# Kernel optimization log

Measured on AMD Instinct MI355X. Metric: run time of the kernel, lower is better.

Reference implementation:

```python
import jax, jax.numpy as jnp
import numpy as np

B, S, D, H = 2, 2048, 1024, 16
HD = D // H  # head_dim = 64


def setup_inputs() -> dict:
    key = jax.random.key(0)
    ks = jax.random.split(key, 10)
    s = 1.0 / np.sqrt(D)
    # causal mask: 0 on/below diagonal, -inf above (matches masked_fill(mask == -inf))
    neg_inf = jnp.float32(-jnp.inf)
    mask = jnp.where(jnp.tril(jnp.ones((S, S), dtype=bool)), 0.0, neg_inf).astype(jnp.float32)
    return {
        "x": jax.random.normal(ks[0], (B, S, D), dtype=jnp.float32),
        "mask": mask,
        "Wq": jax.random.uniform(ks[1], (D, D), jnp.float32, -s, s),
        "bq": jax.random.uniform(ks[2], (D,), jnp.float32, -s, s),
        "Wk": jax.random.uniform(ks[3], (D, D), jnp.float32, -s, s),
        "bk": jax.random.uniform(ks[4], (D,), jnp.float32, -s, s),
        "Wv": jax.random.uniform(ks[5], (D, D), jnp.float32, -s, s),
        "bv": jax.random.uniform(ks[6], (D,), jnp.float32, -s, s),
        "Wo": jax.random.uniform(ks[7], (D, D), jnp.float32, -s, s),
        "bo": jax.random.uniform(ks[8], (D,), jnp.float32, -s, s),
    }


def reference(x, mask, Wq, bq, Wk, bk, Wv, bv, Wo, bo):
    b, s, d = x.shape
    scale = jnp.float32(HD) ** 0.5
    # qkv projections (torch Linear: y = x W^T + b), split into heads: [b, H, s, hd]
    q = (x @ Wq.T + bq).reshape(b, s, H, HD).transpose(0, 2, 1, 3)
    k = (x @ Wk.T + bk).reshape(b, s, H, HD).transpose(0, 2, 1, 3)
    v = (x @ Wv.T + bv).reshape(b, s, H, HD).transpose(0, 2, 1, 3)
    scores = jnp.einsum("bhqd,bhkd->bhqk", q, k) / scale
    scores = jnp.where(mask[None, None] == -jnp.inf, -jnp.inf, scores)
    attn = jax.nn.softmax(scores, axis=-1)
    # dropout(p=0.1) is identity in eval mode
    ctx = jnp.einsum("bhqk,bhkd->bhqd", attn, v)
    ctx = ctx.transpose(0, 2, 1, 3).reshape(b, s, d)
    return ctx @ Wo.T + bo
```

## Files before the change

kernel.cpp:

```cpp
#include <hip/hip_runtime.h>
#include <hip/hip_bf16.h>
#include <cmath>

#define S_ 2048
#define D_ 1024
#define H_ 16
#define HD_ 64
#define GM 4096
#define GN 1024
#define GK 1024
#define QSCALE 0.1803368801111f
#define THR2   11.5415603f

typedef __attribute__((ext_vector_type(4))) float f32x4;
typedef __attribute__((ext_vector_type(8))) short bf16x8;
typedef __attribute__((ext_vector_type(4))) short bf16x4;

__device__ __forceinline__ short f2bf(float f) {
    union { float f; unsigned u; } x; x.f = f;
    unsigned r = x.u + 0x7fffu + ((x.u >> 16) & 1u);
    return (short)(r >> 16);
}
__device__ __forceinline__ short bftrunc(float f) {
    union { float f; unsigned u; } x; x.f = f;
    return (short)(x.u >> 16);
}
__device__ __forceinline__ void gload16(const short* g, short* l) {
    __builtin_amdgcn_global_load_lds((const __attribute__((address_space(1))) void*)g,
                                     (__attribute__((address_space(3))) void*)l, 16, 0, 0);
}

__global__ __launch_bounds__(256) void cvt_all(
    const float* __restrict__ x,
    const float* __restrict__ w0, const float* __restrict__ w1,
    const float* __restrict__ w2, const float* __restrict__ w3,
    short* __restrict__ xb, short* __restrict__ Wb)
{
    const int bid = blockIdx.x;
    const float* src; short* dst; int loc;
    if (bid < 2048) { src = x; dst = xb; loc = bid; }
    else {
        int wsel = (bid - 2048) >> 9, wb = (bid - 2048) & 511;
        src = wsel == 0 ? w0 : wsel == 1 ? w1 : wsel == 2 ? w2 : w3;
        dst = Wb + ((size_t)wsel << 20);
        loc = wb;
    }
    int id = loc * 256 + threadIdx.x;
    const float* s = src + (size_t)id * 8;
    f32x4 a = *(const f32x4*)s;
    f32x4 b = *(const f32x4*)(s + 4);
    bf16x8 h;
    h[0] = f2bf(a[0]); h[1] = f2bf(a[1]); h[2] = f2bf(a[2]); h[3] = f2bf(a[3]);
    h[4] = f2bf(b[0]); h[5] = f2bf(b[1]); h[6] = f2bf(b[2]); h[7] = f2bf(b[3]);
    *(bf16x8*)(dst + (size_t)id * 8) = h;
}

__global__ __launch_bounds__(256) void gemm_qkv(
    const short* __restrict__ A, const short* __restrict__ W3,
    const float* __restrict__ bq, const float* __restrict__ bk, const float* __restrict__ bv,
    short* __restrict__ Qb, short* __restrict__ Kb, short* __restrict__ Vt)
{
    __shared__ short SMEM[17408];
    short* As = SMEM;
    short* Bs = SMEM + 8192;
    const int t = threadIdx.x, lane = t & 63, w = t >> 6;
    const int bid = blockIdx.x;
    const int xcd = bid & 7, idx = bid >> 3;
    const int ntile = idx % 24, mloc = idx / 24;
    const int m0 = (xcd * 4 + mloc) * 128;
    const int n0g = ntile * 128;
    const int wr = (w >> 1) * 64, wc = (w & 1) * 64;
    const int fr = lane & 15, g = lane >> 4;
    const int srow = lane >> 3;
    const int gslot = (lane & 7) ^ srow;
    const int rbase = w * 32;

    f32x4 acc[4][4] = {};

    for (int kt = 0; kt < GK; kt += 64) {
        __syncthreads();
        #pragma unroll
        for (int i = 0; i < 4; ++i) {
            int row = rbase + i * 8 + srow;
            gload16(A  + (size_t)(m0 + row) * GK + kt + gslot * 8, &As[(rbase + i * 8) * 64]);
            gload16(W3 + (size_t)(n0g + row) * GK + kt + gslot * 8, &Bs[(rbase + i * 8) * 64]);
        }
        __syncthreads();
        #pragma unroll
        for (int ks = 0; ks < 2; ++ks) {
            bf16x8 af[4], bf_[4];
            #pragma unroll
            for (int mb = 0; mb < 4; ++mb) {
                int row = wr + mb * 16 + fr;
                af[mb] = *(const bf16x8*)((const char*)As + row * 128 + (((ks * 4 + g) ^ (row & 7)) << 4));
            }
            #pragma unroll
            for (int nb = 0; nb < 4; ++nb) {
                int row = wc + nb * 16 + fr;
                bf_[nb] = *(const bf16x8*)((const char*)Bs + row * 128 + (((ks * 4 + g) ^ (row & 7)) << 4));
            }
            #pragma unroll
            for (int mb = 0; mb < 4; ++mb)
                #pragma unroll
                for (int nb = 0; nb < 4; ++nb)
                    acc[mb][nb] = __builtin_amdgcn_mfma_f32_16x16x32_bf16(
                        af[mb], bf_[nb], acc[mb][nb], 0, 0, 0);
        }
    }

    const int seg = n0g >> 10, nn = n0g & 1023;
    if (seg == 2) {
        __syncthreads();
        short* Cs = SMEM;
        #pragma unroll
        for (int mb = 0; mb < 4; ++mb)
            #pragma unroll
            for (int nb = 0; nb < 4; ++nb) {
                int cl = wc + nb * 16 + fr;
                int rl_ = wr + mb * 16 + g * 4;
                float bvv = bv[nn + cl];
                bf16x4 hv;
                #pragma unroll
                for (int r = 0; r < 4; ++r) hv[r] = f2bf(acc[mb][nb][r] + bvv);
                *(bf16x4*)(Cs + cl * 136 + rl_) = hv;
            }
        __syncthreads();
        const int b = m0 >> 11;
        const int s_base = m0 & 2047;
        #pragma unroll
        for (int p = 0; p < 8; ++p) {
            int id = t + p * 256;
            int cl = id >> 4, ch = id & 15;
            int n = nn + cl;
            int h = n >> 6, d = n & 63;
            bf16x8 v = *(const bf16x8*)(Cs + cl * 136 + ch * 8);
            *(bf16x8*)(Vt + ((size_t)((b * 16 + h) * 64 + d)) * S_ + s_base + ch * 8) = v;
        }
    } else {
        const float* bp = seg ? bk : bq;
        short* dst = seg ? Kb : Qb;
        const float sc = seg ? 1.0f : QSCALE;
        #pragma unroll
        for (int mb = 0; mb < 4; ++mb)
            #pragma unroll
            for (int nb = 0; nb < 4; ++nb) {
                int grow = m0 + wr + mb * 16 + g * 4;
                int gcol = nn + wc + nb * 16 + fr;
                float bvv = bp[gcol];
                #pragma unroll
                for (int r = 0; r < 4; ++r)
                    dst[(size_t)(grow + r) * GN + gcol] = f2bf((acc[mb][nb][r] + bvv) * sc);
            }
    }
}

__global__ __launch_bounds__(256) void gemm_o(
    const short* __restrict__ A, const short* __restrict__ W,
    const float* __restrict__ bias, float* __restrict__ C)
{
    __shared__ short As[2][8192];
    __shared__ short Bs[2][8192];
    const int t = threadIdx.x, lane = t & 63, w = t >> 6;
    const int bid = blockIdx.x;
    const int xcd = bid & 7, wk = bid >> 3;
    const int m0 = (xcd * 4 + (wk & 3)) * 128;
    const int n0 = (wk >> 2) * 128;
    const int wr = (w >> 1) * 64, wc = (w & 1) * 64;
    const int fr = lane & 15, g = lane >> 4;
    const int srow = lane >> 3;
    const int gslot = (lane & 7) ^ srow;
    const int rbase = w * 32;

    f32x4 acc[4][4] = {};

    #pragma unroll
    for (int i = 0; i < 4; ++i) {
        int row = rbase + i * 8 + srow;
        gload16(A + (size_t)(m0 + row) * GK + gslot * 8, &As[0][(rbase + i * 8) * 64]);
        gload16(W + (size_t)(n0 + row) * GK + gslot * 8, &Bs[0][(rbase + i * 8) * 64]);
    }
    __syncthreads();

    int cur = 0;
    for (int t64 = 0; t64 < 16; ++t64) {
        if (t64 < 15) {
            int kt = (t64 + 1) * 64;
            #pragma unroll
            for (int i = 0; i < 4; ++i) {
                int row = rbase + i * 8 + srow;
                gload16(A + (size_t)(m0 + row) * GK + kt + gslot * 8, &As[cur ^ 1][(rbase + i * 8) * 64]);
                gload16(W + (size_t)(n0 + row) * GK + kt + gslot * 8, &Bs[cur ^ 1][(rbase + i * 8) * 64]);
            }
        }
        #pragma unroll
        for (int ks = 0; ks < 2; ++ks) {
            bf16x8 af[4], bf_[4];
            #pragma unroll
            for (int mb = 0; mb < 4; ++mb) {
                int row = wr + mb * 16 + fr;
                af[mb] = *(const bf16x8*)((const char*)&As[cur][0] + row * 128 + (((ks * 4 + g) ^ (row & 7)) << 4));
            }
            #pragma unroll
            for (int nb = 0; nb < 4; ++nb) {
                int row = wc + nb * 16 + fr;
                bf_[nb] = *(const bf16x8*)((const char*)&Bs[cur][0] + row * 128 + (((ks * 4 + g) ^ (row & 7)) << 4));
            }
            #pragma unroll
            for (int mb = 0; mb < 4; ++mb)
                #pragma unroll
                for (int nb = 0; nb < 4; ++nb)
                    acc[mb][nb] = __builtin_amdgcn_mfma_f32_16x16x32_bf16(
                        af[mb], bf_[nb], acc[mb][nb], 0, 0, 0);
        }
        __syncthreads();
        cur ^= 1;
    }

    #pragma unroll
    for (int mb = 0; mb < 4; ++mb)
        #pragma unroll
        for (int nb = 0; nb < 4; ++nb) {
            int grow = m0 + wr + mb * 16 + g * 4;
            int gcol = n0 + wc + nb * 16 + fr;
            float bvv = bias[gcol];
            #pragma unroll
            for (int r = 0; r < 4; ++r)
                C[(size_t)(grow + r) * GN + gcol] = acc[mb][nb][r] + bvv;
        }
}

__global__ __launch_bounds__(256) void attn_fwd_bf16(
    const short* __restrict__ Qb, const short* __restrict__ Kb,
    const short* __restrict__ Vtb, short* __restrict__ Ob)
{
    __shared__ short SK[2][4096];
    __shared__ short SVT[2][4096];
    __shared__ short SP[4][1024];

    const int t = threadIdx.x, lane = t & 63, w = t >> 6;
    const int g = lane >> 4, fr = lane & 15;
    const int bid = blockIdx.x;
    const int xcd = bid & 7, idx = bid >> 3;
    const int bh = xcd * 4 + (idx & 3);
    const int qt = 31 - (idx >> 2);
    const int b = bh >> 4, h = bh & 15;
    const int q0 = qt * 64;
    const int wq0 = w * 16;
    const int nt = qt + 1;

    bf16x8 qf[2];
    #pragma unroll
    for (int ks = 0; ks < 2; ++ks)
        qf[ks] = *(const bf16x8*)(Qb + (size_t)(b * S_ + q0 + wq0 + fr) * D_
                                  + h * 64 + ks * 32 + g * 8);

    const int srow8 = lane >> 3;
    const short* ksrc[2];
    const short* vsrc[2];
    short* kd0[2]; short* kd1[2]; short* vd0[2]; short* vd1[2];
    #pragma unroll
    for (int i = 0; i < 2; ++i) {
        int row = w * 16 + i * 8 + srow8;
        int gsl = (lane & 7) ^ (row & 7);
        ksrc[i] = Kb + (size_t)(b * S_ + row) * D_ + h * 64 + gsl * 8;
        vsrc[i] = Vtb + (size_t)(bh * 64 + row) * S_ + gsl * 8;
        kd0[i] = &SK[0][(w * 16 + i * 8) * 64];  kd1[i] = &SK[1][(w * 16 + i * 8) * 64];
        vd0[i] = &SVT[0][(w * 16 + i * 8) * 64]; vd1[i] = &SVT[1][(w * 16 + i * 8) * 64];
    }
    short* SPw = &SP[w][0];
    const int qsw = fr & 7;

    #pragma unroll
    for (int i = 0; i < 2; ++i) {
        gload16(ksrc[i], kd0[i]);
        gload16(vsrc[i], vd0[i]);
    }
    __syncthreads();

    f32x4 Oacc[4] = {};
    float m2 = -1e30f, lsum = 0.f;
    int cur = 0;

    for (int kt = 0; kt < nt; ++kt) {
        if (kt + 1 < nt) {
            const size_t ko = (size_t)(kt + 1) * 64 * D_;
            const int vo = (kt + 1) * 64;
            if (cur) {
                #pragma unroll
                for (int i = 0; i < 2; ++i) { gload16(ksrc[i] + ko, kd0[i]); gload16(vsrc[i] + vo, vd0[i]); }
            } else {
                #pragma unroll
                for (int i = 0; i < 2; ++i) { gload16(ksrc[i] + ko, kd1[i]); gload16(vsrc[i] + vo, vd1[i]); }
            }
        }
        const char* SKc = (const char*)(cur ? &SK[1][0] : &SK[0][0]);
        const char* SVc = (const char*)(cur ? &SVT[1][0] : &SVT[0][0]);

        f32x4 sacc[4] = {};
        #pragma unroll
        for (int ks = 0; ks < 2; ++ks) {
            #pragma unroll
            for (int mk = 0; mk < 4; ++mk) {
                int row = mk * 16 + fr;
                bf16x8 kf = *(const bf16x8*)(SKc + row * 128 + (((ks * 4 + g) ^ (row & 7)) << 4));
                sacc[mk] = __builtin_amdgcn_mfma_f32_16x16x32_bf16(kf, qf[ks], sacc[mk], 0, 0, 0);
            }
        }
        if (kt == qt) {
            #pragma unroll
            for (int mk = 0; mk < 4; ++mk)
                #pragma unroll
                for (int r = 0; r < 4; ++r)
                    if (mk * 16 + g * 4 + r > wq0 + fr) sacc[mk][r] = -1e30f;
        }

        float rm = -1e30f;
        #pragma unroll
        for (int mk = 0; mk < 4; ++mk)
            #pragma unroll
            for (int r = 0; r < 4; ++r) rm = fmaxf(rm, sacc[mk][r]);
        rm = fmaxf(rm, __shfl_xor(rm, 16));
        rm = fmaxf(rm, __shfl_xor(rm, 32));
        if (rm > m2 + THR2) {
            float resc = exp2f(m2 - rm);
            m2 = rm;
            lsum *= resc;
            #pragma unroll
            for (int md = 0; md < 4; ++md)
                #pragma unroll
                for (int r = 0; r < 4; ++r) Oacc[md][r] *= resc;
        }
        float ps = 0.f;
        #pragma unroll
        for (int mk = 0; mk < 4; ++mk) {
            bf16x4 pk;
            #pragma unroll
            for (int r = 0; r < 4; ++r) {
                float pe = exp2f(sacc[mk][r] - m2);
                ps += pe;
                pk[r] = bftrunc(pe);
            }
            int k = mk * 16 + g * 4;
            *(bf16x4*)((char*)SPw + fr * 128 + (((k >> 3) ^ qsw) << 4) + ((k & 7) << 1)) = pk;
        }
        ps += __shfl_xor(ps, 16);
        ps += __shfl_xor(ps, 32);
        lsum += ps;

        #pragma unroll
        for (int ks = 0; ks < 2; ++ks) {
            bf16x8 pf = *(const bf16x8*)((const char*)SPw + fr * 128 + (((ks * 4 + g) ^ qsw) << 4));
            #pragma unroll
            for (int md = 0; md < 4; ++md) {
                int row = md * 16 + fr;
                bf16x8 vf = *(const bf16x8*)(SVc + row * 128 + (((ks * 4 + g) ^ (row & 7)) << 4));
                Oacc[md] = __builtin_amdgcn_mfma_f32_16x16x32_bf16(vf, pf, Oacc[md], 0, 0, 0);
            }
        }
        __syncthreads();
        cur ^= 1;
    }

    const float rl = 1.f / lsum;
    const size_t orow = (size_t)(b * S_ + q0 + wq0 + fr) * D_ + h * 64;
    #pragma unroll
    for (int md = 0; md < 4; ++md) {
        bf16x4 ov;
        #pragma unroll
        for (int r = 0; r < 4; ++r) ov[r] = f2bf(Oacc[md][r] * rl);
        *(bf16x4*)(Ob + orow + md * 16 + g * 4) = ov;
    }
}

extern "C" void kernel_launch(void* const* d_in, const int* in_sizes, int n_in,
                              void* d_out, int out_size, void* d_ws, size_t ws_size,
                              hipStream_t stream)
{
    const float* x  = (const float*)d_in[0];
    const float* Wq = (const float*)d_in[2];
    const float* bq = (const float*)d_in[3];
    const float* Wk = (const float*)d_in[4];
    const float* bk = (const float*)d_in[5];
    const float* Wv = (const float*)d_in[6];
    const float* bv = (const float*)d_in[7];
    const float* Wo = (const float*)d_in[8];
    const float* bo = (const float*)d_in[9];
    float* out = (float*)d_out;

    const size_t MD = (size_t)GM * D_;
    short* xb = (short*)d_ws;
    short* Wb = xb + MD;
    short* Qb = Wb + 4 * (size_t)D_ * D_;
    short* Kb = Qb + MD;
    short* Vt = Kb + MD;
    short* Ob = Vt + MD;

    dim3 blk(256);
    cvt_all<<<dim3(4096), blk, 0, stream>>>(x, Wq, Wk, Wv, Wo, xb, Wb);
    gemm_qkv<<<dim3(768), blk, 0, stream>>>(xb, Wb, bq, bk, bv, Qb, Kb, Vt);
    attn_fwd_bf16<<<dim3(1024), blk, 0, stream>>>(Qb, Kb, Vt, Ob);
    gemm_o<<<dim3(256), blk, 0, stream>>>(Ob, Wb + 3 * (size_t)D_ * D_, bo, out);
}
```

Before: 122.1 us.

## Double-buffer QKV GEMM shared-memory tiles with prefetch of next K-slice

Restructures the QKV projection GEMM main loop to use two shared-memory buffers with a K-tile of 32 instead of a single buffer with K-tile 64. The next tile's global-to-LDS loads are issued before the MFMAs on the current tile, so load latency can overlap compute, and only one barrier per iteration is needed. The swizzle pattern is adapted to the 64-byte row pitch. In exchange there are twice as many iterations with smaller tiles, and the trailing barrier before the epilogue is removed because the loop now ends with one.

Result: slower. 124.7 us (+2.1%).

```diff
diff --git a/kernel.cpp b/kernel.cpp
--- a/kernel.cpp
+++ b/kernel.cpp
@@ -61,8 +61,6 @@
     short* __restrict__ Qb, short* __restrict__ Kb, short* __restrict__ Vt)
 {
     __shared__ short SMEM[17408];
-    short* As = SMEM;
-    short* Bs = SMEM + 8192;
     const int t = threadIdx.x, lane = t & 63, w = t >> 6;
     const int bid = blockIdx.x;
     const int xcd = bid & 7, idx = bid >> 3;
@@ -71,46 +69,58 @@
     const int n0g = ntile * 128;
     const int wr = (w >> 1) * 64, wc = (w & 1) * 64;
     const int fr = lane & 15, g = lane >> 4;
-    const int srow = lane >> 3;
-    const int gslot = (lane & 7) ^ srow;
-    const int rbase = w * 32;
+    const int r8 = lane >> 2, sl = lane & 3;
+    const int gsl = sl ^ ((r8 >> 1) & 3);
+    const int fsw = (fr >> 1) & 3;
 
     f32x4 acc[4][4] = {};
 
-    for (int kt = 0; kt < GK; kt += 64) {
+    #pragma unroll
+    for (int i = 0; i < 2; ++i) {
+        int rb = w * 32 + i * 16;
+        gload16(A  + (size_t)(m0 + rb + r8) * GK + gsl * 8, SMEM + rb * 32);
+        gload16(W3 + (size_t)(n0g + rb + r8) * GK + gsl * 8, SMEM + 4096 + rb * 32);
+    }
+    __syncthreads();
+
+    int cur = 0;
+    for (int t32 = 0; t32 < 32; ++t32) {
+        if (t32 < 31) {
+            int kt = (t32 + 1) * 32;
+            short* Ad = SMEM + (cur ? 0 : 8192);
+            short* Bd = SMEM + (cur ? 4096 : 12288);
+            #pragma unroll
+            for (int i = 0; i < 2; ++i) {
+                int rb = w * 32 + i * 16;
+                gload16(A  + (size_t)(m0 + rb + r8) * GK + kt + gsl * 8, Ad + rb * 32);
+                gload16(W3 + (size_t)(n0g + rb + r8) * GK + kt + gsl * 8, Bd + rb * 32);
+            }
+        }
+        const char* Asc = (const char*)(SMEM + (cur ? 8192 : 0));
+        const char* Bsc = (const char*)(SMEM + (cur ? 12288 : 4096));
+        bf16x8 af[4], bf_[4];
+        #pragma unroll
+        for (int mb = 0; mb < 4; ++mb) {
+            int row = wr + mb * 16 + fr;
+            af[mb] = *(const bf16x8*)(Asc + row * 64 + ((g ^ fsw) << 4));
+        }
+        #pragma unroll
+        for (int nb = 0; nb < 4; ++nb) {
+            int row = wc + nb * 16 + fr;
+            bf_[nb] = *(const bf16x8*)(Bsc + row * 64 + ((g ^ fsw) << 4));
+        }
+        #pragma unroll
+        for (int mb = 0; mb < 4; ++mb)
+            #pragma unroll
+            for (int nb = 0; nb < 4; ++nb)
+                acc[mb][nb] = __builtin_amdgcn_mfma_f32_16x16x32_bf16(
+                    af[mb], bf_[nb], acc[mb][nb], 0, 0, 0);
         __syncthreads();
-        #pragma unroll
-        for (int i = 0; i < 4; ++i) {
-            int row = rbase + i * 8 + srow;
-            gload16(A  + (size_t)(m0 + row) * GK + kt + gslot * 8, &As[(rbase + i * 8) * 64]);
-            gload16(W3 + (size_t)(n0g + row) * GK + kt + gslot * 8, &Bs[(rbase + i * 8) * 64]);
-        }
-        __syncthreads();
-        #pragma unroll
-        for (int ks = 0; ks < 2; ++ks) {
-            bf16x8 af[4], bf_[4];
-            #pragma unroll
-            for (int mb = 0; mb < 4; ++mb) {
-                int row = wr + mb * 16 + fr;
-                af[mb] = *(const bf16x8*)((const char*)As + row * 128 + (((ks * 4 + g) ^ (row & 7)) << 4));
-            }
-            #pragma unroll
-            for (int nb = 0; nb < 4; ++nb) {
-                int row = wc + nb * 16 + fr;
-                bf_[nb] = *(const bf16x8*)((const char*)Bs + row * 128 + (((ks * 4 + g) ^ (row & 7)) << 4));
-            }
-            #pragma unroll
-            for (int mb = 0; mb < 4; ++mb)
-                #pragma unroll
-                for (int nb = 0; nb < 4; ++nb)
-                    acc[mb][nb] = __builtin_amdgcn_mfma_f32_16x16x32_bf16(
-                        af[mb], bf_[nb], acc[mb][nb], 0, 0, 0);
-        }
+        cur ^= 1;
     }
 
     const int seg = n0g >> 10, nn = n0g & 1023;
     if (seg == 2) {
-        __syncthreads();
         short* Cs = SMEM;
         #pragma unroll
         for (int mb = 0; mb < 4; ++mb)
```
